# Optimization experiments

Hardware: AMD Instinct MI355X
Metric: run time of the kernel (lower is better)

The kernel has to match this reference:

```python
import jax, jax.numpy as jnp
import numpy as np

# dims: N sentences, L tokens each, M=2 memory slots/sentence, D hidden, H heads
N, L, M, D, H, FF, V, P, LAYERS = 4, 256, 2, 768, 12, 3072, 32000, 1024, 4
DH = D // H


def setup_inputs() -> dict:
    key = jax.random.key(0)
    ks = jax.random.split(key, 20)
    s = 0.02
    inp = {
        'input_ids': jax.random.randint(ks[0], (N, L), 0, V),
        'memory': jax.random.normal(ks[1], (N, M, D), jnp.float32),
        'emb_table': jax.random.normal(ks[2], (V, D), jnp.float32) * s,
        'pos_table': jax.random.normal(ks[3], (P + 2, D), jnp.float32) * s,
        'Wq': jax.random.normal(ks[4], (LAYERS, D, D), jnp.float32) * s,
        'bq': jnp.zeros((LAYERS, D), jnp.float32),
        'Wk': jax.random.normal(ks[5], (LAYERS, D, D), jnp.float32) * s,
        'bk': jnp.zeros((LAYERS, D), jnp.float32),
        'Wv': jax.random.normal(ks[6], (LAYERS, D, D), jnp.float32) * s,
        'bv': jnp.zeros((LAYERS, D), jnp.float32),
        'W1': jax.random.normal(ks[7], (LAYERS, D, FF), jnp.float32) * s,
        'b1': jnp.zeros((LAYERS, FF), jnp.float32),
        'W2': jax.random.normal(ks[8], (LAYERS, FF, D), jnp.float32) * s,
        'b2': jnp.zeros((LAYERS, D), jnp.float32),
        'g1': jnp.ones((LAYERS, D), jnp.float32),
        'be1': jnp.zeros((LAYERS, D), jnp.float32),
        'g2': jnp.ones((LAYERS, D), jnp.float32),
        'be2': jnp.zeros((LAYERS, D), jnp.float32),
    }
    return inp


def _layer_norm(x, g, b):
    mu = jnp.mean(x, axis=-1, keepdims=True)
    var = jnp.mean((x - mu) ** 2, axis=-1, keepdims=True)
    return (x - mu) / jnp.sqrt(var + 1e-5) * g + b


def _encoder(input_ids, memory, emb_table, pos_table, Wq, bq, Wk, bk, Wv, bv,
             W1, b1, W2, b2, g1, be1, g2, be2):
    base = N * M            # token rows start here in the packed input
    T = base + N * L        # total rows (memory rows + token rows)
    Kk = M + L              # keys per query (own memory + own tokens)

    # position embeddings: memory rows get pos (p % M); tokens get id_pos + M
    mem_pos = jnp.tile(jnp.arange(M), N)                    # (N*M,)
    mem = memory.reshape(N * M, D) + pos_table[mem_pos]
    fwd_pos = jnp.tile(jnp.arange(L) + M, N)                # (N*L,)
    tok = emb_table[input_ids.reshape(-1)] + pos_table[fwd_pos]
    x = jnp.concatenate([mem, tok], axis=0)                 # (T, D)

    # per-sentence key set: its M memory rows then its L token rows
    key_pos = jnp.concatenate([
        jnp.arange(N)[:, None] * M + jnp.arange(M)[None, :],
        base + jnp.arange(N)[:, None] * L + jnp.arange(L)[None, :],
    ], axis=1)                                              # (N, Kk)
    sent = jnp.concatenate([jnp.repeat(jnp.arange(N), M),
                            jnp.repeat(jnp.arange(N), L)])  # (T,)
    gidx = key_pos[sent]                                    # (T, Kk)
    # equal-length sentences => the additive mask built by the torch code is
    # all zeros (key_len == max_key_len for every row), so it is omitted.

    scale = 1.0 / np.sqrt(DH)
    for i in range(LAYERS):
        # K/V are linear row-wise, so project once on all rows then gather
        # (identical math to projecting the gathered tgt, without T-fold GEMM)
        q = (x @ Wq[i] + bq[i]).reshape(T, H, DH)
        kf = (x @ Wk[i] + bk[i]).reshape(T, H, DH)
        vf = (x @ Wv[i] + bv[i]).reshape(T, H, DH)
        kg = kf[gidx]                                       # (T, Kk, H, DH)
        vg = vf[gidx]
        scores = jnp.einsum('thd,tkhd->thk', q, kg) * scale
        probs = jax.nn.softmax(scores, axis=-1)
        ctx = jnp.einsum('thk,tkhd->thd', probs, vg).reshape(T, D)
        x = _layer_norm(x + ctx, g1[i], be1[i])
        h = jax.nn.gelu(x @ W1[i] + b1[i], approximate=False)
        x = _layer_norm(x + h @ W2[i] + b2[i], g2[i], be2[i])

    ret = key_pos[:, M:]                                    # (N, L) token rows
    return x[ret]                                           # (N, L, D)


def reference(input_ids, memory, emb_table, pos_table, Wq, bq, Wk, bk, Wv, bv,
              W1, b1, W2, b2, g1, be1, g2, be2):
    return _encoder(input_ids, memory, emb_table, pos_table, Wq, bq, Wk, bk,
                    Wv, bv, W1, b1, W2, b2, g1, be1, g2, be2)
```

## Files before the change

kernel.cpp:

```cpp
#include <hip/hip_runtime.h>
#include <hip/hip_bf16.h>
#include <math.h>

#define N_      4
#define L_      256
#define M_      2
#define D_      768
#define H_      12
#define FF_     3072
#define DH_     64
#define LAYERS_ 4
#define BASE_   8
#define T_      1032
#define TP_     1088
#define KK_     258
#define QS_     2304
#define PS_     264

typedef __bf16 bf16x8 __attribute__((ext_vector_type(8)));
typedef float  f32x4  __attribute__((ext_vector_type(4)));

#define PPL_      6336
#define PP_WEND_  25344
#define PP_B_END_ 25380
#define PP_TOTAL_ 26412
#define PP_UP_    7404

struct KP {
  const int* ids; const float* memory; const float* emb; const float* pos;
  const float* Wq; const float* bq; const float* Wk; const float* bk;
  const float* Wv; const float* bv; const float* W1; const float* b1;
  const float* W2; const float* b2; const float* g1; const float* be1;
  const float* g2; const float* be2;
  float *x, *cb, *bqkv;
  __hip_bfloat16 *xb, *qkvb, *vtb, *hbb, *Wqkvt, *W1t, *W2t;
  float* out;
};

struct __align__(16) SharedG {
  __hip_bfloat16 As[2][2][64][32];
  __hip_bfloat16 Bs[2][2][64][32];
};

__device__ __forceinline__ void async_load16(const __hip_bfloat16* g, __hip_bfloat16* l) {
  __builtin_amdgcn_global_load_lds(
      (const __attribute__((address_space(1))) unsigned int*)g,
      (__attribute__((address_space(3))) unsigned int*)l, 16, 0, 0);
}

__device__ __forceinline__ void pp_unit(int bid, const KP& p, float (&tile)[32][33]) {
  const int tid = threadIdx.x;
  const float* src;
  __hip_bfloat16* dst;
  int K, N, bx, by;

  if (bid < PP_WEND_) {
    int l = bid / PPL_, r = bid - l * PPL_;
    if (r < 1728) {
      int which = r / 576, t = r - which * 576;
      by = t / 24; bx = t - by * 24;
      src = (which == 0 ? p.Wq : which == 1 ? p.Wk : p.Wv) + (size_t)l * D_ * D_;
      dst = p.Wqkvt + (size_t)l * QS_ * D_ + (size_t)which * D_ * D_;
      K = D_; N = D_;
    } else if (r < 4032) {
      int t = r - 1728;
      by = t / 96; bx = t - by * 96;
      src = p.W1 + (size_t)l * D_ * FF_;
      dst = p.W1t + (size_t)l * FF_ * D_;
      K = D_; N = FF_;
    } else {
      int t = r - 4032;
      by = t / 24; bx = t - by * 24;
      src = p.W2 + (size_t)l * FF_ * D_;
      dst = p.W2t + (size_t)l * D_ * FF_;
      K = FF_; N = D_;
    }
  } else if (bid < PP_B_END_) {
    int i = (bid - PP_WEND_) * 256 + tid;
    int l = i / QS_, j = i - l * QS_;
    float v;
    if (j < D_)            v = p.bq[l * D_ + j];
    else if (j < 2 * D_)   v = p.bk[l * D_ + (j - D_)];
    else                   v = p.bv[l * D_ + (j - 2 * D_)];
    p.bqkv[i] = v;
    return;
  } else {
    int row = bid - PP_B_END_;
    const float *s2, *pp;
    if (row < BASE_) {
      s2 = p.memory + (long long)row * D_;
      pp = p.pos + (row & 1) * D_;
    } else {
      int i = row - BASE_;
      int tok = p.ids[i];
      s2 = p.emb + (long long)tok * D_;
      pp = p.pos + (M_ + (i & (L_ - 1))) * D_;
    }
    for (int d = tid; d < D_; d += 256) {
      float v = s2[d] + pp[d];
      p.x[(long long)row * D_ + d]  = v;
      p.xb[(long long)row * D_ + d] = __float2bfloat16(v);
    }
    return;
  }

  const int k0 = by * 32, n0 = bx * 32;
  const int r = tid >> 5, c = tid & 31;
  #pragma unroll
  for (int i = 0; i < 4; ++i)
    tile[r + i * 8][c] = src[(size_t)(k0 + r + i * 8) * N + n0 + c];
  __syncthreads();
  #pragma unroll
  for (int i = 0; i < 4; ++i)
    dst[(size_t)(n0 + r + i * 8) * K + k0 + c] = __float2bfloat16(tile[c][r + i * 8]);
}

template <int ACT, int WF32, int WBF16, int WVT, int NSPLIT>
__device__ __forceinline__ void gemm_tile(
    int bx, int by, int bz,
    const __hip_bfloat16* __restrict__ A, const __hip_bfloat16* __restrict__ Bt,
    const float* __restrict__ bias, float* __restrict__ C,
    __hip_bfloat16* __restrict__ Cb, __hip_bfloat16* __restrict__ vt,
    int N, int Ktot, SharedG& sg) {
  const int tid  = threadIdx.x;
  const int lane = tid & 63, wid = tid >> 6;
  const int ln   = lane & 15, qd = lane >> 4;
  const int wm   = wid >> 1, wn = wid & 1;

  const int K = Ktot / NSPLIT;
  const size_t koff = (size_t)bz * K;
  const size_t arow = (size_t)(by * 64 + wid * 16 + (lane >> 2)) * Ktot + koff + (lane & 3) * 8;
  const size_t brow = (size_t)(bx * 64 + wid * 16 + (lane >> 2)) * Ktot + koff + (lane & 3) * 8;

  f32x4 acc[2][2] = {};

#define STAGE_(b, k0)                                                         \
  do {                                                                        \
    _Pragma("unroll")                                                         \
    for (int s_ = 0; s_ < 2; ++s_) {                                          \
      async_load16(A  + arow + (k0) + s_ * 32, &sg.As[b][s_][wid * 16][0]);   \
      async_load16(Bt + brow + (k0) + s_ * 32, &sg.Bs[b][s_][wid * 16][0]);   \
    }                                                                         \
  } while (0)

  STAGE_(0, 0);
  __syncthreads();
  int buf = 0;
  for (int k0 = 0; k0 < K; k0 += 64) {
    if (k0 + 64 < K) STAGE_(buf ^ 1, k0 + 64);
    #pragma unroll
    for (int s = 0; s < 2; ++s) {
      bf16x8 a0 = *(const bf16x8*)&sg.As[buf][s][wm * 32 + ln][qd * 8];
      bf16x8 a1 = *(const bf16x8*)&sg.As[buf][s][wm * 32 + 16 + ln][qd * 8];
      bf16x8 b0 = *(const bf16x8*)&sg.Bs[buf][s][wn * 32 + ln][qd * 8];
      bf16x8 b1 = *(const bf16x8*)&sg.Bs[buf][s][wn * 32 + 16 + ln][qd * 8];
      acc[0][0] = __builtin_amdgcn_mfma_f32_16x16x32_bf16(a0, b0, acc[0][0], 0, 0, 0);
      acc[0][1] = __builtin_amdgcn_mfma_f32_16x16x32_bf16(a0, b1, acc[0][1], 0, 0, 0);
      acc[1][0] = __builtin_amdgcn_mfma_f32_16x16x32_bf16(a1, b0, acc[1][0], 0, 0, 0);
      acc[1][1] = __builtin_amdgcn_mfma_f32_16x16x32_bf16(a1, b1, acc[1][1], 0, 0, 0);
    }
    __syncthreads();
    buf ^= 1;
  }
#undef STAGE_

  #pragma unroll
  for (int mt = 0; mt < 2; ++mt) {
    #pragma unroll
    for (int nt = 0; nt < 2; ++nt) {
      const int col = bx * 64 + wn * 32 + nt * 16 + ln;
      const float bv = (NSPLIT == 1 || bz == 0) ? bias[col] : 0.f;
      #pragma unroll
      for (int i = 0; i < 4; ++i) {
        const int row = by * 64 + wm * 32 + mt * 16 + qd * 4 + i;
        float v = acc[mt][nt][i] + bv;
        if (ACT) v = 0.5f * v * (1.f + erff(v * 0.70710678118654752f));
        if (WF32)
          C[(size_t)bz * TP_ * N + (size_t)row * N + col] = v;
        if (WVT) {
          if (col < 2 * D_) Cb[(size_t)row * N + col] = __float2bfloat16(v);
          else              vt[(size_t)(col - 2 * D_) * TP_ + row] = __float2bfloat16(v);
        } else if (WBF16) {
          Cb[(size_t)row * N + col] = __float2bfloat16(v);
        }
      }
    }
  }
}

__global__ __launch_bounds__(256) void pp_k(KP p) {
  __shared__ float tile[32][33];
  int bid = blockIdx.x;
  if (bid >= PPL_) bid = bid - PPL_ + PP_WEND_;
  pp_unit(bid, p, tile);
}

__global__ __launch_bounds__(256, 4) void gemm_qkv_k(KP p, int l) {
  __shared__ SharedG sg;
  gemm_tile<0, 0, 1, 1, 1>(blockIdx.x, blockIdx.y, 0, p.xb,
                           p.Wqkvt + (size_t)l * QS_ * D_, p.bqkv + l * QS_,
                           nullptr, p.qkvb, p.vtb, QS_, D_, sg);
}

__global__ __launch_bounds__(256, 4) void gemm_ffn1_k(KP p, int l) {
  __shared__ union { SharedG g; float tile[32][33]; } sh;
  const int bid = blockIdx.x;
  if (bid < 48 * 17) {
    gemm_tile<1, 0, 1, 0, 1>(bid % 48, bid / 48, 0, p.xb,
                             p.W1t + (size_t)l * FF_ * D_, p.b1 + l * FF_,
                             nullptr, p.hbb, nullptr, FF_, D_, sh.g);
  } else {
    pp_unit(bid - 48 * 17 + (l + 1) * PPL_, p, sh.tile);
  }
}

__global__ __launch_bounds__(256, 4) void gemm_ffn2_k(KP p, int l) {
  __shared__ SharedG sg;
  gemm_tile<0, 1, 0, 0, 2>(blockIdx.x, blockIdx.y, blockIdx.z, p.hbb,
                           p.W2t + (size_t)l * D_ * FF_, p.b2 + l * D_,
                           p.cb, nullptr, nullptr, D_, FF_, sg);
}

__global__ __launch_bounds__(256) void attn_k(KP p) {
  __shared__ __align__(16) __hip_bfloat16 Ps[64][PS_];
  const __hip_bfloat16* qkv = p.qkvb;
  const __hip_bfloat16* vtb = p.vtb;
  float* ctx = p.cb;
  const int qt = blockIdx.x, h = blockIdx.y, b = blockIdx.z;
  const int tid = threadIdx.x;
  const int w = tid >> 6, lane = tid & 63, ln = lane & 15, qd = lane >> 4;

  bf16x8 aq0, aq1;
  {
    int j = qt * 64 + w * 16 + ln;
    int tok = (j < 256) ? (BASE_ + b * L_ + j)
            : ((j < KK_) ? (b * M_ + (j - 256)) : (b * M_));
    const __hip_bfloat16* qp = qkv + (size_t)tok * QS_ + h * DH_ + qd * 8;
    aq0 = *(const bf16x8*)qp;
    aq1 = *(const bf16x8*)(qp + 32);
  }

  f32x4 sa[17];
  #pragma unroll
  for (int nt = 0; nt < 17; ++nt) sa[nt] = (f32x4){0.f, 0.f, 0.f, 0.f};
  #pragma unroll
  for (int nt = 0; nt < 17; ++nt) {
    int key = nt * 16 + ln;
    int ktok = (key < 256) ? (BASE_ + b * L_ + key)
             : ((key < KK_) ? (b * M_ + (key - 256)) : (b * M_));
    const __hip_bfloat16* kp = qkv + (size_t)ktok * QS_ + D_ + h * DH_ + qd * 8;
    bf16x8 b0 = *(const bf16x8*)kp;
    bf16x8 b1 = *(const bf16x8*)(kp + 32);
    sa[nt] = __builtin_amdgcn_mfma_f32_16x16x32_bf16(aq0, b0, sa[nt], 0, 0, 0);
    sa[nt] = __builtin_amdgcn_mfma_f32_16x16x32_bf16(aq1, b1, sa[nt], 0, 0, 0);
  }

  #pragma unroll
  for (int i = 0; i < 4; ++i) {
    float v[17];
    #pragma unroll
    for (int nt = 0; nt < 17; ++nt) v[nt] = sa[nt][i] * 0.125f;
    float mx = -1e30f;
    #pragma unroll
    for (int nt = 0; nt < 16; ++nt) mx = fmaxf(mx, v[nt]);
    if (ln < 2) mx = fmaxf(mx, v[16]);
    #pragma unroll
    for (int m = 1; m < 16; m <<= 1) mx = fmaxf(mx, __shfl_xor(mx, m));
    float sum = 0.f;
    #pragma unroll
    for (int nt = 0; nt < 17; ++nt) {
      float e = (nt == 16 && ln >= 2) ? 0.f : __expf(v[nt] - mx);
      v[nt] = e;
      sum += e;
    }
    #pragma unroll
    for (int m = 1; m < 16; m <<= 1) sum += __shfl_xor(sum, m);
    float is = 1.f / sum;
    const int row = w * 16 + qd * 4 + i;
    #pragma unroll
    for (int nt = 0; nt < 17; ++nt)
      if (nt < 16 || ln < 2)
        Ps[row][nt * 16 + ln] = __float2bfloat16(v[nt] * is);
  }

  f32x4 oa[4] = {};
  #pragma unroll
  for (int k0 = 0; k0 < 8; ++k0) {
    bf16x8 ap = *(const bf16x8*)&Ps[w * 16 + ln][k0 * 32 + qd * 8];
    #pragma unroll
    for (int nt = 0; nt < 4; ++nt) {
      const __hip_bfloat16* vp = vtb + (size_t)(h * DH_ + nt * 16 + ln) * TP_
                               + BASE_ + b * L_ + k0 * 32 + qd * 8;
      bf16x8 bv = *(const bf16x8*)vp;
      oa[nt] = __builtin_amdgcn_mfma_f32_16x16x32_bf16(ap, bv, oa[nt], 0, 0, 0);
    }
  }
  {
    float p0[4], p1[4];
    #pragma unroll
    for (int i = 0; i < 4; ++i) {
      p0[i] = __bfloat162float(Ps[w * 16 + qd * 4 + i][256]);
      p1[i] = __bfloat162float(Ps[w * 16 + qd * 4 + i][257]);
    }
    #pragma unroll
    for (int nt = 0; nt < 4; ++nt) {
      const __hip_bfloat16* vp = vtb + (size_t)(h * DH_ + nt * 16 + ln) * TP_ + b * M_;
      float v0 = __bfloat162float(vp[0]);
      float v1 = __bfloat162float(vp[1]);
      #pragma unroll
      for (int i = 0; i < 4; ++i) oa[nt][i] += p0[i] * v0 + p1[i] * v1;
    }
  }

  #pragma unroll
  for (int i = 0; i < 4; ++i) {
    int j = qt * 64 + w * 16 + qd * 4 + i;
    if (j < KK_) {
      int tok = (j < 256) ? (BASE_ + b * L_ + j) : (b * M_ + (j - 256));
      #pragma unroll
      for (int nt = 0; nt < 4; ++nt)
        ctx[(size_t)tok * D_ + h * DH_ + nt * 16 + ln] = oa[nt][i];
    }
  }
}

template <int NS>
__global__ __launch_bounds__(256) void ln_k(KP p, int l, int last) {
  __shared__ float sred[4];
  __shared__ float sbc;
  const float* g = (NS == 1) ? p.g1 + l * D_ : p.g2 + l * D_;
  const float* b = (NS == 1) ? p.be1 + l * D_ : p.be2 + l * D_;
  const int t = blockIdx.x, tid = threadIdx.x;
  float y[3];
  float s = 0.f;
  #pragma unroll
  for (int i = 0; i < 3; ++i) {
    int d = tid + i * 256;
    float v = p.x[(long long)t * D_ + d];
    #pragma unroll
    for (int s2 = 0; s2 < NS; ++s2)
      v += p.cb[(size_t)s2 * TP_ * D_ + (long long)t * D_ + d];
    y[i] = v;
    s += v;
  }
  #pragma unroll
  for (int o = 32; o > 0; o >>= 1) s += __shfl_down(s, o);
  if ((tid & 63) == 0) sred[tid >> 6] = s;
  __syncthreads();
  if (tid == 0) sbc = (sred[0] + sred[1] + sred[2] + sred[3]) * (1.f / D_);
  __syncthreads();
  const float mu = sbc;
  __syncthreads();
  float vs = 0.f;
  #pragma unroll
  for (int i = 0; i < 3; ++i) { float d = y[i] - mu; vs += d * d; }
  #pragma unroll
  for (int o = 32; o > 0; o >>= 1) vs += __shfl_down(vs, o);
  if ((tid & 63) == 0) sred[tid >> 6] = vs;
  __syncthreads();
  if (tid == 0) sbc = (sred[0] + sred[1] + sred[2] + sred[3]) * (1.f / D_);
  __syncthreads();
  const float inv = rsqrtf(sbc + 1e-5f);
  #pragma unroll
  for (int i = 0; i < 3; ++i) {
    int d = tid + i * 256;
    float v = (y[i] - mu) * inv * g[d] + b[d];
    p.x[(long long)t * D_ + d]  = v;
    p.xb[(long long)t * D_ + d] = __float2bfloat16(v);
    if (last && t >= BASE_)
      p.out[(size_t)(t - BASE_) * D_ + d] = v;
  }
}

extern "C" void kernel_launch(void* const* d_in, const int* in_sizes, int n_in,
                              void* d_out, int out_size, void* d_ws, size_t ws_size,
                              hipStream_t stream) {
  KP p;
  p.ids    = (const int*)  d_in[0];
  p.memory = (const float*)d_in[1];
  p.emb    = (const float*)d_in[2];
  p.pos    = (const float*)d_in[3];
  p.Wq     = (const float*)d_in[4];
  p.bq     = (const float*)d_in[5];
  p.Wk     = (const float*)d_in[6];
  p.bk     = (const float*)d_in[7];
  p.Wv     = (const float*)d_in[8];
  p.bv     = (const float*)d_in[9];
  p.W1     = (const float*)d_in[10];
  p.b1     = (const float*)d_in[11];
  p.W2     = (const float*)d_in[12];
  p.b2     = (const float*)d_in[13];
  p.g1     = (const float*)d_in[14];
  p.be1    = (const float*)d_in[15];
  p.g2     = (const float*)d_in[16];
  p.be2    = (const float*)d_in[17];
  p.out    = (float*)d_out;

  char* w = (char*)d_ws;
  p.x     = (float*)w;                     w += (size_t)TP_ * D_ * 4;
  p.cb    = (float*)w;                     w += (size_t)2 * TP_ * D_ * 4;
  p.bqkv  = (float*)w;                     w += (size_t)LAYERS_ * QS_ * 4;
  p.xb    = (__hip_bfloat16*)w;            w += (size_t)TP_ * D_ * 2;
  p.qkvb  = (__hip_bfloat16*)w;            w += (size_t)TP_ * QS_ * 2;
  p.vtb   = (__hip_bfloat16*)w;            w += (size_t)D_ * TP_ * 2;
  p.hbb   = (__hip_bfloat16*)w;            w += (size_t)TP_ * FF_ * 2;
  p.Wqkvt = (__hip_bfloat16*)w;            w += (size_t)LAYERS_ * QS_ * D_ * 2;
  p.W1t   = (__hip_bfloat16*)w;            w += (size_t)LAYERS_ * FF_ * D_ * 2;
  p.W2t   = (__hip_bfloat16*)w;            w += (size_t)LAYERS_ * D_ * FF_ * 2;

  pp_k<<<PP_UP_, 256, 0, stream>>>(p);

  for (int i = 0; i < LAYERS_; ++i) {
    gemm_qkv_k<<<dim3(QS_ / 64, TP_ / 64), 256, 0, stream>>>(p, i);
    attn_k<<<dim3(5, H_, N_), 256, 0, stream>>>(p);
    ln_k<1><<<T_, 256, 0, stream>>>(p, i, 0);
    gemm_ffn1_k<<<48 * 17 + (i < LAYERS_ - 1 ? PPL_ : 0), 256, 0, stream>>>(p, i);
    gemm_ffn2_k<<<dim3(D_ / 64, TP_ / 64, 2), 256, 0, stream>>>(p, i);
    ln_k<2><<<T_, 256, 0, stream>>>(p, i, i == LAYERS_ - 1 ? 1 : 0);
  }
}
```

Baseline: 519.3 us.

## Replace LDS-staged GEMM with direct register loads and compile-time K

The GEMM tile no longer stages A and B through LDS with async global-to-LDS loads and block barriers. Each wave now loads its MFMA fragments straight from global memory into registers, prefetching one k-step ahead, and K is a template constant so the loop can unroll. This removes LDS traffic and __syncthreads, but every wave re-reads fragments another wave in the block shares, and each load is a strided 16-byte read with little coalescing. The occupancy hint in the launch bounds is also dropped.

Result: slower. 842.9 us (+62.3%).

```diff
diff --git a/kernel.cpp b/kernel.cpp
--- a/kernel.cpp
+++ b/kernel.cpp
@@ -36,17 +36,6 @@
   __hip_bfloat16 *xb, *qkvb, *vtb, *hbb, *Wqkvt, *W1t, *W2t;
   float* out;
 };
-
-struct __align__(16) SharedG {
-  __hip_bfloat16 As[2][2][64][32];
-  __hip_bfloat16 Bs[2][2][64][32];
-};
-
-__device__ __forceinline__ void async_load16(const __hip_bfloat16* g, __hip_bfloat16* l) {
-  __builtin_amdgcn_global_load_lds(
-      (const __attribute__((address_space(1))) unsigned int*)g,
-      (__attribute__((address_space(3))) unsigned int*)l, 16, 0, 0);
-}
 
 __device__ __forceinline__ void pp_unit(int bid, const KP& p, float (&tile)[32][33]) {
   const int tid = threadIdx.x;
@@ -115,54 +104,45 @@
     dst[(size_t)(n0 + r + i * 8) * K + k0 + c] = __float2bfloat16(tile[c][r + i * 8]);
 }
 
-template <int ACT, int WF32, int WBF16, int WVT, int NSPLIT>
+template <int ACT, int WF32, int WBF16, int WVT, int KTOT, int NSPLIT>
 __device__ __forceinline__ void gemm_tile(
     int bx, int by, int bz,
     const __hip_bfloat16* __restrict__ A, const __hip_bfloat16* __restrict__ Bt,
     const float* __restrict__ bias, float* __restrict__ C,
-    __hip_bfloat16* __restrict__ Cb, __hip_bfloat16* __restrict__ vt,
-    int N, int Ktot, SharedG& sg) {
+    __hip_bfloat16* __restrict__ Cb, __hip_bfloat16* __restrict__ vt, int N) {
   const int tid  = threadIdx.x;
   const int lane = tid & 63, wid = tid >> 6;
   const int ln   = lane & 15, qd = lane >> 4;
   const int wm   = wid >> 1, wn = wid & 1;
 
-  const int K = Ktot / NSPLIT;
+  constexpr int K = KTOT / NSPLIT;
   const size_t koff = (size_t)bz * K;
-  const size_t arow = (size_t)(by * 64 + wid * 16 + (lane >> 2)) * Ktot + koff + (lane & 3) * 8;
-  const size_t brow = (size_t)(bx * 64 + wid * 16 + (lane >> 2)) * Ktot + koff + (lane & 3) * 8;
+  const __hip_bfloat16* ap0 = A  + (size_t)(by * 64 + wm * 32 + ln) * KTOT + koff + qd * 8;
+  const __hip_bfloat16* ap1 = ap0 + (size_t)16 * KTOT;
+  const __hip_bfloat16* bp0 = Bt + (size_t)(bx * 64 + wn * 32 + ln) * KTOT + koff + qd * 8;
+  const __hip_bfloat16* bp1 = bp0 + (size_t)16 * KTOT;
 
   f32x4 acc[2][2] = {};
 
-#define STAGE_(b, k0)                                                         \
-  do {                                                                        \
-    _Pragma("unroll")                                                         \
-    for (int s_ = 0; s_ < 2; ++s_) {                                          \
-      async_load16(A  + arow + (k0) + s_ * 32, &sg.As[b][s_][wid * 16][0]);   \
-      async_load16(Bt + brow + (k0) + s_ * 32, &sg.Bs[b][s_][wid * 16][0]);   \
-    }                                                                         \
-  } while (0)
-
-  STAGE_(0, 0);
-  __syncthreads();
-  int buf = 0;
-  for (int k0 = 0; k0 < K; k0 += 64) {
-    if (k0 + 64 < K) STAGE_(buf ^ 1, k0 + 64);
-    #pragma unroll
-    for (int s = 0; s < 2; ++s) {
-      bf16x8 a0 = *(const bf16x8*)&sg.As[buf][s][wm * 32 + ln][qd * 8];
-      bf16x8 a1 = *(const bf16x8*)&sg.As[buf][s][wm * 32 + 16 + ln][qd * 8];
-      bf16x8 b0 = *(const bf16x8*)&sg.Bs[buf][s][wn * 32 + ln][qd * 8];
-      bf16x8 b1 = *(const bf16x8*)&sg.Bs[buf][s][wn * 32 + 16 + ln][qd * 8];
-      acc[0][0] = __builtin_amdgcn_mfma_f32_16x16x32_bf16(a0, b0, acc[0][0], 0, 0, 0);
-      acc[0][1] = __builtin_amdgcn_mfma_f32_16x16x32_bf16(a0, b1, acc[0][1], 0, 0, 0);
-      acc[1][0] = __builtin_amdgcn_mfma_f32_16x16x32_bf16(a1, b0, acc[1][0], 0, 0, 0);
-      acc[1][1] = __builtin_amdgcn_mfma_f32_16x16x32_bf16(a1, b1, acc[1][1], 0, 0, 0);
-    }
-    __syncthreads();
-    buf ^= 1;
-  }
-#undef STAGE_
+  bf16x8 a0 = *(const bf16x8*)(ap0);
+  bf16x8 a1 = *(const bf16x8*)(ap1);
+  bf16x8 b0 = *(const bf16x8*)(bp0);
+  bf16x8 b1 = *(const bf16x8*)(bp1);
+  #pragma unroll 4
+  for (int k0 = 0; k0 < K; k0 += 32) {
+    bf16x8 na0, na1, nb0, nb1;
+    if (k0 + 32 < K) {
+      na0 = *(const bf16x8*)(ap0 + k0 + 32);
+      na1 = *(const bf16x8*)(ap1 + k0 + 32);
+      nb0 = *(const bf16x8*)(bp0 + k0 + 32);
+      nb1 = *(const bf16x8*)(bp1 + k0 + 32);
+    }
+    acc[0][0] = __builtin_amdgcn_mfma_f32_16x16x32_bf16(a0, b0, acc[0][0], 0, 0, 0);
+    acc[0][1] = __builtin_amdgcn_mfma_f32_16x16x32_bf16(a0, b1, acc[0][1], 0, 0, 0);
+    acc[1][0] = __builtin_amdgcn_mfma_f32_16x16x32_bf16(a1, b0, acc[1][0], 0, 0, 0);
+    acc[1][1] = __builtin_amdgcn_mfma_f32_16x16x32_bf16(a1, b1, acc[1][1], 0, 0, 0);
+    a0 = na0; a1 = na1; b0 = nb0; b1 = nb1;
+  }
 
   #pragma unroll
   for (int mt = 0; mt < 2; ++mt) {
@@ -195,30 +175,28 @@
   pp_unit(bid, p, tile);
 }
 
-__global__ __launch_bounds__(256, 4) void gemm_qkv_k(KP p, int l) {
-  __shared__ SharedG sg;
-  gemm_tile<0, 0, 1, 1, 1>(blockIdx.x, blockIdx.y, 0, p.xb,
-                           p.Wqkvt + (size_t)l * QS_ * D_, p.bqkv + l * QS_,
-                           nullptr, p.qkvb, p.vtb, QS_, D_, sg);
-}
-
-__global__ __launch_bounds__(256, 4) void gemm_ffn1_k(KP p, int l) {
-  __shared__ union { SharedG g; float tile[32][33]; } sh;
+__global__ __launch_bounds__(256) void gemm_qkv_k(KP p, int l) {
+  gemm_tile<0, 0, 1, 1, D_, 1>(blockIdx.x, blockIdx.y, 0, p.xb,
+                               p.Wqkvt + (size_t)l * QS_ * D_, p.bqkv + l * QS_,
+                               nullptr, p.qkvb, p.vtb, QS_);
+}
+
+__global__ __launch_bounds__(256) void gemm_ffn1_k(KP p, int l) {
+  __shared__ float tile[32][33];
   const int bid = blockIdx.x;
   if (bid < 48 * 17) {
-    gemm_tile<1, 0, 1, 0, 1>(bid % 48, bid / 48, 0, p.xb,
-                             p.W1t + (size_t)l * FF_ * D_, p.b1 + l * FF_,
-                             nullptr, p.hbb, nullptr, FF_, D_, sh.g);
+    gemm_tile<1, 0, 1, 0, D_, 1>(bid % 48, bid / 48, 0, p.xb,
+                                 p.W1t + (size_t)l * FF_ * D_, p.b1 + l * FF_,
+                                 nullptr, p.hbb, nullptr, FF_);
   } else {
-    pp_unit(bid - 48 * 17 + (l + 1) * PPL_, p, sh.tile);
-  }
-}
-
-__global__ __launch_bounds__(256, 4) void gemm_ffn2_k(KP p, int l) {
-  __shared__ SharedG sg;
-  gemm_tile<0, 1, 0, 0, 2>(blockIdx.x, blockIdx.y, blockIdx.z, p.hbb,
-                           p.W2t + (size_t)l * D_ * FF_, p.b2 + l * D_,
-                           p.cb, nullptr, nullptr, D_, FF_, sg);
+    pp_unit(bid - 48 * 17 + (l + 1) * PPL_, p, tile);
+  }
+}
+
+__global__ __launch_bounds__(256) void gemm_ffn2_k(KP p, int l) {
+  gemm_tile<0, 1, 0, 0, FF_, 2>(blockIdx.x, blockIdx.y, blockIdx.z, p.hbb,
+                                p.W2t + (size_t)l * D_ * FF_, p.b2 + l * D_,
+                                p.cb, nullptr, nullptr, D_);
 }
 
 __global__ __launch_bounds__(256) void attn_k(KP p) {
```
